# Kernel optimization log

Measured on AMD Instinct MI355X. Metric: run time of the kernel, lower is better.

## Reference

```python
import jax, jax.numpy as jnp
import numpy as np

D = 2            # stalk dimension d
FD = 3           # final_d = d + 1 (add_lp=True, add_hp=False)
HID = 32         # hidden_channels
N_NODES = 50000
E0 = 200000      # undirected edges; directed edge list has 2*E0 entries (second half reversed)
IN_CH = 128
OUT_CH = 32
N_LAYERS = 2
PSIZE = D * (D + 1) // 2  # cayley param size per edge


def _spectral_normalize(W, iters=20):
    # torch spectral_norm: power iteration with detached u, v; sigma = u^T W v
    u = jnp.full((W.shape[0],), 1.0 / np.sqrt(W.shape[0]), W.dtype)
    def body(_, u):
        v = W.T @ u
        v = v / (jnp.linalg.norm(v) + 1e-12)
        u2 = W @ v
        return u2 / (jnp.linalg.norm(u2) + 1e-12)
    u = jax.lax.fori_loop(0, iters, body, u)
    u = jax.lax.stop_gradient(u)
    v = jax.lax.stop_gradient(W.T @ u)
    v = v / (jnp.linalg.norm(v) + 1e-12)
    return W / (u @ W @ v)


def _cayley(p):
    # p: [E, PSIZE] lower-tri params -> skew A -> orthogonal Q = (I - A)^{-1}(I + A)
    E = p.shape[0]
    r, c = jnp.tril_indices(D)
    M = jnp.zeros((E, D, D), p.dtype).at[:, r, c].set(p)
    A = M - jnp.swapaxes(M, 1, 2)
    I = jnp.eye(D, dtype=p.dtype)
    return jnp.linalg.solve(I[None] - A, I[None] + A)


def setup_inputs() -> dict:
    key = jax.random.key(0)
    ks = jax.random.split(key, 8)
    src = jax.random.randint(ks[0], (E0,), 0, N_NODES)
    dst = jax.random.randint(ks[1], (E0,), 0, N_NODES)
    # symmetric directed edge list; edge j and edge j+E0 are reverses of each other
    edge_index = jnp.concatenate([jnp.stack([src, dst]), jnp.stack([dst, src])], axis=1)
    x = jax.random.normal(ks[2], (N_NODES, IN_CH), jnp.float32)
    s = 0.02
    W1 = jax.random.normal(ks[3], (FD * HID, IN_CH), jnp.float32) * s
    b1 = jnp.zeros((FD * HID,), jnp.float32)
    W2 = jax.random.normal(ks[4], (OUT_CH, FD * HID), jnp.float32) * s
    b2 = jnp.zeros((OUT_CH,), jnp.float32)
    W_left = jnp.tile(jnp.eye(FD, dtype=jnp.float32)[None], (N_LAYERS, 1, 1))  # init eye per torch
    W_right = jax.random.normal(ks[5], (N_LAYERS, HID, HID), jnp.float32) / np.sqrt(HID)
    eps = jnp.zeros((N_LAYERS, FD, 1), jnp.float32)
    W_sheaf = jax.random.normal(ks[6], (N_LAYERS, PSIZE, 2 * FD * HID), jnp.float32) * s
    W_wt = jax.random.normal(ks[7], (N_LAYERS, 1, 2 * FD * HID), jnp.float32) * s
    return {"x": x, "edge_index": edge_index, "W1": W1, "b1": b1, "W2": W2, "b2": b2,
            "W_left": W_left, "W_right": W_right, "eps": eps, "W_sheaf": W_sheaf, "W_wt": W_wt}


def reference(x, edge_index, W1, b1, W2, b2, W_left, W_right, eps, W_sheaf, W_wt):
    N = x.shape[0]
    row, col = edge_index[0], edge_index[1]
    e0 = row.shape[0] // 2
    rev = jnp.concatenate([jnp.arange(e0) + e0, jnp.arange(e0)])  # reverse-edge index
    # lin1 + ELU (dropouts = 0 in eval)
    h = jax.nn.elu(x @ W1.T + b1)                 # [N, FD*HID]
    xc = h.reshape(N * FD, HID)                   # [N*FD, HID]
    x0 = xc
    for layer in range(N_LAYERS):
        # --- sheaf learner + edge weight learner (gather endpoint features) ---
        xn = xc.reshape(N, FD * HID)
        cat = jnp.concatenate([xn[row], xn[col]], axis=-1)   # [2*E0, 2*FD*HID]
        p = jnp.tanh(cat @ W_sheaf[layer].T)                 # sheaf map params [2*E0, PSIZE]
        wdir = jax.nn.sigmoid(cat @ W_wt[layer].T)[:, 0]
        w = wdir * wdir[rev]                                 # symmetric edge weight
        # --- normalized connection (bundle) Laplacian ---
        Q = _cayley(p)                                       # per-edge orthogonal maps
        T = jnp.einsum('eij,eik->ejk', Q, Q[rev])            # transport F_u^T F_v
        w2 = w * w
        deg = jax.ops.segment_sum(w2, row, num_segments=N)
        dinv = jnp.where(deg > 0, jax.lax.rsqrt(jnp.maximum(deg, 1e-30)), 0.0)
        cnorm = w2 * dinv[row] * dinv[col]                   # [2*E0]
        # --- left / right weights (spectral-normalized) ---
        Wl = _spectral_normalize(W_left[layer])
        Wr = _spectral_normalize(W_right[layer])
        y = xc.reshape(N, FD, HID)
        y = jnp.einsum('ef,nfh->neh', Wl, y)                 # mix stalk dims
        y = jnp.einsum('neh,ch->nec', y, Wr)                 # mix channels
        # --- apply block-sparse Laplacian: Lx[u] = x[u] - sum_e c_e B_e x[v] ---
        yv = y[col]                                          # gather  [2*E0, FD, HID]
        tv = jnp.concatenate([jnp.einsum('eij,ejh->eih', T, yv[:, :D]), yv[:, D:]], axis=1)
        agg = jax.ops.segment_sum(cnorm[:, None, None] * tv, row, num_segments=N)
        diag = jnp.where(deg > 0, 1.0, 0.0)[:, None, None]
        z = jax.nn.elu((diag * y - agg).reshape(N * FD, HID))
        # --- epsilon-gated residual ---
        coeff = jnp.tile(1.0 + jnp.tanh(eps[layer]), (N, 1))  # [N*FD, 1]
        x0 = coeff * x0 - z
        xc = x0
    return xc.reshape(N, FD * HID) @ W2.T + b2
```

## Files before the change

kernel.cpp:

```cpp
#include <hip/hip_runtime.h>

#define NN 50000
#define E0 200000
#define E2 400000
#define NGROUPS ((NN + 7) / 8)
#define NCHUNK  ((NN + 255) / 256)
#define NTILES  ((NN + 63) / 64)
#define EB      ((E2 + 255) / 256)

typedef __attribute__((ext_vector_type(8))) short short8;
typedef __attribute__((ext_vector_type(4))) float f32x4;

__device__ __forceinline__ float eluf(float x) { return x > 0.0f ? x : expm1f(x); }
__device__ __forceinline__ float fsig(float x) { return 1.0f / (1.0f + __expf(-x)); }
__device__ __forceinline__ float ftanh(float x) {
    float e = __expf(-2.0f * x);
    return (1.0f - e) / (1.0f + e);
}
__device__ __forceinline__ unsigned rne_bf16(float x) {
    unsigned u = __float_as_uint(x);
    return (u + 0x7fffu + ((u >> 16) & 1u)) >> 16;
}

__device__ __forceinline__ void spectral_block(int l, const float* __restrict__ Wl_in,
                                               const float* __restrict__ Wr_in,
                                               float* __restrict__ Wl_out, float* __restrict__ Wr_out) {
    __shared__ float W[32 * 33];
    __shared__ float sscal;
    int t = threadIdx.x;
    for (int i = t; i < 1024; i += 256) W[(i >> 5) * 33 + (i & 31)] = Wr_in[l * 1024 + i];
    __syncthreads();
    if (t < 32) {
        float u = 0.17677669529663688f;
        for (int it = 0; it < 20; ++it) {
            float v = 0.f;
#pragma unroll 8
            for (int r = 0; r < 32; ++r) v = fmaf(W[r * 33 + t], __shfl(u, r, 32), v);
            float s = v * v;
#pragma unroll
            for (int off = 16; off; off >>= 1) s += __shfl_xor(s, off, 32);
            v *= 1.0f / (sqrtf(s) + 1e-12f);
            float u2 = 0.f;
#pragma unroll 8
            for (int c = 0; c < 32; ++c) u2 = fmaf(W[t * 33 + c], __shfl(v, c, 32), u2);
            s = u2 * u2;
#pragma unroll
            for (int off = 16; off; off >>= 1) s += __shfl_xor(s, off, 32);
            u = u2 * (1.0f / (sqrtf(s) + 1e-12f));
        }
        float v = 0.f;
#pragma unroll 8
        for (int r = 0; r < 32; ++r) v = fmaf(W[r * 33 + t], __shfl(u, r, 32), v);
        float s = v * v;
#pragma unroll
        for (int off = 16; off; off >>= 1) s += __shfl_xor(s, off, 32);
        if (t == 0) sscal = (sqrtf(s) + 1e-12f) / s;
    } else if (t == 64) {
        float M[9];
        for (int i = 0; i < 9; ++i) M[i] = Wl_in[l * 9 + i];
        float u[3] = {0.5773502691896258f, 0.5773502691896258f, 0.5773502691896258f};
        float v[3], u2[3];
        for (int it = 0; it < 20; ++it) {
            float s = 0;
            for (int c = 0; c < 3; ++c) { v[c] = M[c] * u[0] + M[3 + c] * u[1] + M[6 + c] * u[2]; s += v[c] * v[c]; }
            float inv = 1.0f / (sqrtf(s) + 1e-12f);
            for (int c = 0; c < 3; ++c) v[c] *= inv;
            s = 0;
            for (int r = 0; r < 3; ++r) { u2[r] = M[r * 3] * v[0] + M[r * 3 + 1] * v[1] + M[r * 3 + 2] * v[2]; s += u2[r] * u2[r]; }
            inv = 1.0f / (sqrtf(s) + 1e-12f);
            for (int r = 0; r < 3; ++r) u[r] = u2[r] * inv;
        }
        float s = 0;
        for (int c = 0; c < 3; ++c) { v[c] = M[c] * u[0] + M[3 + c] * u[1] + M[6 + c] * u[2]; s += v[c] * v[c]; }
        float inv = (sqrtf(s) + 1e-12f) / s;
        for (int i = 0; i < 9; ++i) Wl_out[l * 9 + i] = M[i] * inv;
    }
    __syncthreads();
    float invs = sscal;
    for (int i = t; i < 1024; i += 256) Wr_out[l * 1024 + i] = W[(i >> 5) * 33 + (i & 31)] * invs;
}

__global__ __launch_bounds__(256) void k_setup(const float* __restrict__ Wl_in, const float* __restrict__ Wr_in,
                                               float* __restrict__ Wl_out, float* __restrict__ Wr_out,
                                               int* __restrict__ cnt, int* __restrict__ fill,
                                               float* __restrict__ deg0, int* __restrict__ gtotal) {
    if (blockIdx.x < 2) {
        spectral_block((int)blockIdx.x, Wl_in, Wr_in, Wl_out, Wr_out);
        return;
    }
    int i = (blockIdx.x - 2) * 256 + threadIdx.x;
    if (i == 0) *gtotal = 0;
    if (i < NN) { cnt[i] = 0; fill[i] = 0; deg0[i] = 0.0f; }
}

template<int K, int N, int NH, bool ELU, bool HIST>
__global__ __launch_bounds__(256) void k_gemm(const float* __restrict__ X,
                                              const float* __restrict__ W,
                                              const float* __restrict__ bias,
                                              float* __restrict__ out,
                                              const int* __restrict__ row, int* __restrict__ cnt) {
    constexpr int KP = K + 8;
    constexpr int NT = NH / 16;
    constexpr int KS = K / 32;
    constexpr int NHALVES = N / NH;
    __shared__ __align__(16) unsigned short whi[NH * KP];
    __shared__ __align__(16) unsigned short wlo[NH * KP];
    int tid = threadIdx.x;
    if (HIST) {
        for (int e = blockIdx.x * 256 + tid; e < E2; e += gridDim.x * 256)
            atomicAdd(&cnt[row[e]], 1);
    }
    const int ch = blockIdx.x % NHALVES;
    const int tstream = blockIdx.x / NHALVES;
    const int nstreams = gridDim.x / NHALVES;
    for (int i = tid; i < NH * K; i += 256) {
        float v = W[ch * NH * K + i];
        int r = i / K, c = i % K;
        unsigned h = rne_bf16(v);
        whi[r * KP + c] = (unsigned short)h;
        wlo[r * KP + c] = (unsigned short)rne_bf16(v - __uint_as_float(h << 16));
    }
    __syncthreads();
    int wave = tid >> 6, lane = tid & 63;
    int quad = lane >> 4, r16 = lane & 15;
    for (int t = tstream; t < NTILES; t += nstreams) {
        long m = (long)t * 64 + wave * 16 + r16;
        long mc = m < NN ? m : (NN - 1);
        const float* xrow = X + mc * K + quad * 8;
        short8 ah[KS], al[KS];
#pragma unroll
        for (int ks = 0; ks < KS; ++ks) {
            const float4* xp = (const float4*)(xrow + ks * 32);
            float4 p0 = xp[0], p1 = xp[1];
            float xv[8] = {p0.x, p0.y, p0.z, p0.w, p1.x, p1.y, p1.z, p1.w};
#pragma unroll
            for (int j = 0; j < 8; ++j) {
                unsigned h = rne_bf16(xv[j]);
                ah[ks][j] = (short)h;
                al[ks][j] = (short)rne_bf16(xv[j] - __uint_as_float(h << 16));
            }
        }
        long mbase = (long)t * 64 + wave * 16 + quad * 4;
#pragma unroll
        for (int tt = 0; tt < NT; ++tt) {
            f32x4 acc = (f32x4){0.f, 0.f, 0.f, 0.f};
#pragma unroll
            for (int ks = 0; ks < KS; ++ks) {
                int ro = (tt * 16 + r16) * KP + ks * 32 + quad * 8;
                short8 bh = *(const short8*)&whi[ro];
                short8 bl = *(const short8*)&wlo[ro];
                acc = __builtin_amdgcn_mfma_f32_16x16x32_bf16(ah[ks], bh, acc, 0, 0, 0);
                acc = __builtin_amdgcn_mfma_f32_16x16x32_bf16(al[ks], bh, acc, 0, 0, 0);
                acc = __builtin_amdgcn_mfma_f32_16x16x32_bf16(ah[ks], bl, acc, 0, 0, 0);
            }
            int coln = ch * NH + tt * 16 + r16;
            float b = bias[coln];
#pragma unroll
            for (int rr = 0; rr < 4; ++rr) {
                long mm = mbase + rr;
                if (mm < NN) {
                    float v = acc[rr] + b;
                    if (ELU) v = eluf(v);
                    out[mm * N + coln] = v;
                }
            }
        }
    }
}

__global__ __launch_bounds__(256) void k_scan(const int* __restrict__ cnt, int* __restrict__ start,
                                              int* __restrict__ gtotal) {
    __shared__ int s[256];
    __shared__ int soff;
    int b = blockIdx.x, t = threadIdx.x;
    int i = b * 256 + t;
    int v = (i < NN) ? cnt[i] : 0;
    s[t] = v;
    __syncthreads();
    for (int off = 1; off < 256; off <<= 1) {
        int add = (t >= off) ? s[t - off] : 0;
        __syncthreads();
        s[t] += add;
        __syncthreads();
    }
    if (t == 255) soff = atomicAdd(gtotal, s[255]);
    __syncthreads();
    if (i < NN) start[i] = s[t] - v + soff;
}

__global__ __launch_bounds__(256) void k_filly8(const float* __restrict__ xc,
                                                const float* __restrict__ Wl, const float* __restrict__ Wr,
                                                const float* __restrict__ Wsh, const float* __restrict__ Wwt,
                                                unsigned* __restrict__ yA, unsigned short* __restrict__ yB,
                                                float4* __restrict__ proj,
                                                const int* __restrict__ row, const int* __restrict__ start,
                                                int* __restrict__ fill, int* __restrict__ eslot) {
    int tid = threadIdx.x;
    if (blockIdx.x >= NGROUPS) {
        int e = (blockIdx.x - NGROUPS) * 256 + tid;
        if (e < E2) {
            int u = row[e];
            eslot[e] = start[u] + atomicAdd(&fill[u], 1);
        }
        return;
    }
    __shared__ float wrs[32 * 33];
    __shared__ float wls[9];
    __shared__ float xcs[8][96];
    __shared__ float ws1[192], wt[192];
    int n0 = blockIdx.x * 8;
    for (int i = tid; i < 1024; i += 256) wrs[(i >> 5) * 33 + (i & 31)] = Wr[i];
    if (tid < 9) wls[tid] = Wl[tid];
    if (tid < 192) {
        ws1[tid] = Wsh[192 + tid];
        wt[tid]  = Wwt[tid];
    }
    for (int i = tid; i < 192; i += 256) {
        int nd = i / 24, of = (i % 24) * 4;
        *(float4*)&xcs[nd][of] = *(const float4*)&xc[(n0 + nd) * 96 + of];
    }
    __syncthreads();
    int node = tid >> 5, c = tid & 31;
    int n = n0 + node;
    float a1 = 0, a2 = 0, a3 = 0, a4 = 0;
#pragma unroll
    for (int j = 0; j < 3; ++j) {
        int k = j * 32 + c;
        float xv = xcs[node][k];
        a1 = fmaf(xv, ws1[k], a1);
        a2 = fmaf(xv, ws1[96 + k], a2);
        a3 = fmaf(xv, wt[k], a3);
        a4 = fmaf(xv, wt[96 + k], a4);
    }
#pragma unroll
    for (int off = 16; off; off >>= 1) {
        a1 += __shfl_xor(a1, off);
        a2 += __shfl_xor(a2, off);
        a3 += __shfl_xor(a3, off);
        a4 += __shfl_xor(a4, off);
    }
    if (c == 0) proj[n] = make_float4(a1, a2, a3, a4);
    {
        float t0 = 0, t1 = 0, t2 = 0;
        const float* wr = &wrs[c * 33];
        const float* xr = xcs[node];
#pragma unroll
        for (int h = 0; h < 32; ++h) {
            float w = wr[h];
            t0 = fmaf(xr[h], w, t0);
            t1 = fmaf(xr[32 + h], w, t1);
            t2 = fmaf(xr[64 + h], w, t2);
        }
        float o0 = wls[0] * t0 + wls[1] * t1 + wls[2] * t2;
        float o1 = wls[3] * t0 + wls[4] * t1 + wls[5] * t2;
        float o2 = wls[6] * t0 + wls[7] * t1 + wls[8] * t2;
        yA[n * 32 + c] = rne_bf16(o0) | (rne_bf16(o1) << 16);
        yB[n * 32 + c] = (unsigned short)rne_bf16(o2);
    }
}

__global__ __launch_bounds__(256) void k_coef(const int* __restrict__ row, const int* __restrict__ col,
                                              const int* __restrict__ eslot,
                                              const float4* __restrict__ proj,
                                              uint2* __restrict__ meta, float* __restrict__ deg) {
    int e = blockIdx.x * 256 + threadIdx.x;
    if (e >= E0) return;
    int u = row[e], v = col[e];
    float4 pu = proj[u], pv = proj[v];
    float a_e = ftanh(pu.x + pv.y);
    float a_r = ftanh(pv.x + pu.y);
    float wd_e = fsig(pu.z + pv.w);
    float wd_r = fsig(pv.z + pu.w);
    float w = wd_e * wd_r;
    float w2 = w * w;
    float ie = 1.0f / (1.0f + a_e * a_e), ir = 1.0f / (1.0f + a_r * a_r);
    float ce = (1.0f - a_e * a_e) * ie, se = 2.0f * a_e * ie;
    float cr = (1.0f - a_r * a_r) * ir, sr = 2.0f * a_r * ir;
    float C = ce * cr + se * sr;
    float S = ce * sr - se * cr;
    unsigned cb = rne_bf16(C), sb = rne_bf16(S), wb = rne_bf16(w2);
    meta[eslot[e]]      = make_uint2(cb | (sb << 16), (unsigned)v | (wb << 16));
    meta[eslot[e + E0]] = make_uint2(cb | ((sb ^ 0x8000u) << 16), (unsigned)u | (wb << 16));
    atomicAdd(&deg[u], w2);
    atomicAdd(&deg[v], w2);
}

__device__ __forceinline__ void gather_accum(int s0, int ec, int c,
                                             const uint2* __restrict__ meta,
                                             const float* __restrict__ deg, float du,
                                             const unsigned* __restrict__ yA,
                                             const unsigned short* __restrict__ yB,
                                             float4* __restrict__ ecoef,
                                             float& acc0, float& acc1, float& acc2) {
    for (int bs = 0; bs < ec; bs += 32) {
        int nb2 = min(32, ec - bs);
        if (c < nb2) {
            uint2 mt = meta[s0 + bs + c];
            int vj = (int)(mt.y & 0xffffu);
            float w2 = __uint_as_float(mt.y & 0xffff0000u);
            float Cv = __uint_as_float(mt.x << 16);
            float Sv = __uint_as_float(mt.x & 0xffff0000u);
            float dv = deg[vj];
            float dvi = dv > 0.0f ? rsqrtf(fmaxf(dv, 1e-30f)) : 0.0f;
            float cnl = w2 * du * dvi;
            ecoef[c] = make_float4(cnl * Cv, cnl * Sv, cnl, __int_as_float(vj));
        }
        int j4 = nb2 & ~3;
        int j = 0;
        for (; j < j4; j += 4) {
#pragma unroll
            for (int jj = 0; jj < 4; ++jj) {
                float4 e = ecoef[j + jj];
                int v = __float_as_int(e.w);
                unsigned ua = yA[v * 32 + c];
                unsigned ub = (unsigned)yB[v * 32 + c];
                float y0 = __uint_as_float(ua << 16);
                float y1 = __uint_as_float(ua & 0xffff0000u);
                float y2 = __uint_as_float(ub << 16);
                acc0 = fmaf(e.x, y0, acc0);
                acc0 = fmaf(-e.y, y1, acc0);
                acc1 = fmaf(e.y, y0, acc1);
                acc1 = fmaf(e.x, y1, acc1);
                acc2 = fmaf(e.z, y2, acc2);
            }
        }
        for (; j < nb2; ++j) {
            float4 e = ecoef[j];
            int v = __float_as_int(e.w);
            unsigned ua = yA[v * 32 + c];
            unsigned ub = (unsigned)yB[v * 32 + c];
            float y0 = __uint_as_float(ua << 16);
            float y1 = __uint_as_float(ua & 0xffff0000u);
            float y2 = __uint_as_float(ub << 16);
            acc0 = fmaf(e.x, y0, acc0);
            acc0 = fmaf(-e.y, y1, acc0);
            acc1 = fmaf(e.y, y0, acc1);
            acc1 = fmaf(e.x, y1, acc1);
            acc2 = fmaf(e.z, y2, acc2);
        }
    }
}

__global__ __launch_bounds__(256) void k_gatherY(const int* __restrict__ start,
                                                 const int* __restrict__ cnt,
                                                 const uint2* __restrict__ meta,
                                                 const float* __restrict__ deg0,
                                                 const unsigned* __restrict__ yA0,
                                                 const unsigned short* __restrict__ yB0,
                                                 const float* __restrict__ eps,
                                                 float* __restrict__ xc,
                                                 const float* __restrict__ Wl, const float* __restrict__ Wr,
                                                 const float* __restrict__ Wsh, const float* __restrict__ Wwt,
                                                 unsigned* __restrict__ yA1, unsigned short* __restrict__ yB1,
                                                 float4* __restrict__ proj, float* __restrict__ deg1) {
    __shared__ float wrs[32 * 33];
    __shared__ float wls[9];
    __shared__ float xcs[8][96];
    __shared__ float ws1[192], wt[192];
    __shared__ float4 ecoef[8][32];
    int tid = threadIdx.x;
    int node = tid >> 5, c = tid & 31;
    int n = blockIdx.x * 8 + node;
    int s0 = start[n], ec = cnt[n];
    float dn = deg0[n];
    for (int i = tid; i < 1024; i += 256) wrs[(i >> 5) * 33 + (i & 31)] = Wr[i];
    if (tid < 9) wls[tid] = Wl[tid];
    if (tid < 192) {
        ws1[tid] = Wsh[(1 * 3 + 1) * 192 + tid];
        wt[tid]  = Wwt[1 * 192 + tid];
    }
    __syncthreads();
    float du = dn > 0.0f ? rsqrtf(fmaxf(dn, 1e-30f)) : 0.0f;
    float acc0 = 0, acc1 = 0, acc2 = 0;
    gather_accum(s0, ec, c, meta, deg0, du, yA0, yB0, ecoef[node], acc0, acc1, acc2);
    float diag = dn > 0.0f ? 1.0f : 0.0f;
    unsigned ua = yA0[n * 32 + c];
    unsigned ub = (unsigned)yB0[n * 32 + c];
    float oy0 = __uint_as_float(ua << 16);
    float oy1 = __uint_as_float(ua & 0xffff0000u);
    float oy2 = __uint_as_float(ub << 16);
    float c0 = 1.0f + tanhf(eps[0]);
    float c1 = 1.0f + tanhf(eps[1]);
    float c2 = 1.0f + tanhf(eps[2]);
    int base = n * 96 + c;
    float nx0 = c0 * xc[base]      - eluf(diag * oy0 - acc0);
    float nx1 = c1 * xc[base + 32] - eluf(diag * oy1 - acc1);
    float nx2 = c2 * xc[base + 64] - eluf(diag * oy2 - acc2);
    xc[base] = nx0; xc[base + 32] = nx1; xc[base + 64] = nx2;
    if (c == 0) deg1[n] = 0.0f;
    xcs[node][c] = nx0; xcs[node][32 + c] = nx1; xcs[node][64 + c] = nx2;
    float a1 = nx0 * ws1[c] + nx1 * ws1[32 + c] + nx2 * ws1[64 + c];
    float a2 = nx0 * ws1[96 + c] + nx1 * ws1[128 + c] + nx2 * ws1[160 + c];
    float a3 = nx0 * wt[c] + nx1 * wt[32 + c] + nx2 * wt[64 + c];
    float a4 = nx0 * wt[96 + c] + nx1 * wt[128 + c] + nx2 * wt[160 + c];
#pragma unroll
    for (int off = 16; off; off >>= 1) {
        a1 += __shfl_xor(a1, off);
        a2 += __shfl_xor(a2, off);
        a3 += __shfl_xor(a3, off);
        a4 += __shfl_xor(a4, off);
    }
    if (c == 0) proj[n] = make_float4(a1, a2, a3, a4);
    {
        float t0 = 0, t1 = 0, t2 = 0;
        const float* wr = &wrs[c * 33];
        const float* xr = xcs[node];
#pragma unroll
        for (int h = 0; h < 32; ++h) {
            float w = wr[h];
            t0 = fmaf(xr[h], w, t0);
            t1 = fmaf(xr[32 + h], w, t1);
            t2 = fmaf(xr[64 + h], w, t2);
        }
        float o0 = wls[0] * t0 + wls[1] * t1 + wls[2] * t2;
        float o1 = wls[3] * t0 + wls[4] * t1 + wls[5] * t2;
        float o2 = wls[6] * t0 + wls[7] * t1 + wls[8] * t2;
        yA1[n * 32 + c] = rne_bf16(o0) | (rne_bf16(o1) << 16);
        yB1[n * 32 + c] = (unsigned short)rne_bf16(o2);
    }
}

__global__ __launch_bounds__(256) void k_gather(const int* __restrict__ start,
                                                const int* __restrict__ cnt,
                                                const uint2* __restrict__ meta,
                                                const float* __restrict__ deg,
                                                const unsigned* __restrict__ yA,
                                                const unsigned short* __restrict__ yB,
                                                const float* __restrict__ eps,
                                                int layer, float* __restrict__ xc) {
    __shared__ float4 ecoef[8][32];
    int tid = threadIdx.x;
    int node = tid >> 5, c = tid & 31;
    int n = blockIdx.x * 8 + node;
    if (n >= NN) return;
    int s0 = start[n], ec = cnt[n];
    float dn = deg[n];
    float du = dn > 0.0f ? rsqrtf(fmaxf(dn, 1e-30f)) : 0.0f;
    float acc0 = 0, acc1 = 0, acc2 = 0;
    gather_accum(s0, ec, c, meta, deg, du, yA, yB, ecoef[node], acc0, acc1, acc2);
    float diag = dn > 0.0f ? 1.0f : 0.0f;
    unsigned ua = yA[n * 32 + c];
    unsigned ub = (unsigned)yB[n * 32 + c];
    float oy0 = __uint_as_float(ua << 16);
    float oy1 = __uint_as_float(ua & 0xffff0000u);
    float oy2 = __uint_as_float(ub << 16);
    float c0 = 1.0f + tanhf(eps[layer * 3 + 0]);
    float c1 = 1.0f + tanhf(eps[layer * 3 + 1]);
    float c2 = 1.0f + tanhf(eps[layer * 3 + 2]);
    int base = n * 96 + c;
    float z0 = eluf(diag * oy0 - acc0);
    float z1 = eluf(diag * oy1 - acc1);
    float z2 = eluf(diag * oy2 - acc2);
    xc[base]      = c0 * xc[base]      - z0;
    xc[base + 32] = c1 * xc[base + 32] - z1;
    xc[base + 64] = c2 * xc[base + 64] - z2;
}

extern "C" void kernel_launch(void* const* d_in, const int* in_sizes, int n_in,
                              void* d_out, int out_size, void* d_ws, size_t ws_size,
                              hipStream_t stream) {
    const float* x     = (const float*)d_in[0];
    const int*   ei    = (const int*)d_in[1];
    const float* W1    = (const float*)d_in[2];
    const float* b1    = (const float*)d_in[3];
    const float* W2    = (const float*)d_in[4];
    const float* b2    = (const float*)d_in[5];
    const float* Wl    = (const float*)d_in[6];
    const float* Wr    = (const float*)d_in[7];
    const float* eps   = (const float*)d_in[8];
    const float* Wsh   = (const float*)d_in[9];
    const float* Wwt   = (const float*)d_in[10];
    float* out = (float*)d_out;
    const int* row = ei;
    const int* col = ei + E2;

    char* pc = (char*)d_ws;
    float* xc     = (float*)pc;          pc += (size_t)NN * 96 * 4;
    uint2* meta   = (uint2*)pc;          pc += (size_t)E2 * 8;
    unsigned* yA0 = (unsigned*)pc;       pc += (size_t)NN * 32 * 4;
    unsigned* yA1 = (unsigned*)pc;       pc += (size_t)NN * 32 * 4;
    unsigned short* yB0 = (unsigned short*)pc; pc += (size_t)NN * 32 * 2;
    unsigned short* yB1 = (unsigned short*)pc; pc += (size_t)NN * 32 * 2;
    pc = (char*)(((size_t)pc + 15) & ~(size_t)15);
    float4* proj  = (float4*)pc;         pc += (size_t)NN * 16;
    float* deg0   = (float*)pc;          pc += (size_t)NN * 4;
    float* deg1   = (float*)pc;          pc += (size_t)NN * 4;
    float* Wl_n   = (float*)pc;          pc += 32 * 4;
    float* Wr_n   = (float*)pc;          pc += 2048 * 4;
    int* cnt      = (int*)pc;            pc += (size_t)NN * 4;
    int* start    = (int*)pc;            pc += (size_t)NN * 4;
    int* fill     = (int*)pc;            pc += (size_t)NN * 4;
    int* eslot    = (int*)pc;            pc += (size_t)E2 * 4;
    int* gtotal   = (int*)pc;            pc += 4;

    k_setup<<<NCHUNK + 2, 256, 0, stream>>>(Wl, Wr, Wl_n, Wr_n, cnt, fill, deg0, gtotal);
    k_gemm<128, 96, 48, true, true><<<1024, 256, 0, stream>>>(x, W1, b1, xc, row, cnt);
    k_scan<<<NCHUNK, 256, 0, stream>>>(cnt, start, gtotal);
    k_filly8<<<NGROUPS + EB, 256, 0, stream>>>(xc, Wl_n, Wr_n, Wsh, Wwt,
                                               yA0, yB0, proj, row, start, fill, eslot);
    k_coef<<<(E0 + 255) / 256, 256, 0, stream>>>(row, col, eslot, proj, meta, deg0);
    k_gatherY<<<NGROUPS, 256, 0, stream>>>(start, cnt, meta, deg0, yA0, yB0, eps, xc,
                                           Wl_n + 9, Wr_n + 1024, Wsh, Wwt, yA1, yB1, proj, deg1);
    k_coef<<<(E0 + 255) / 256, 256, 0, stream>>>(row, col, eslot, proj, meta, deg1);
    k_gather<<<NGROUPS, 256, 0, stream>>>(start, cnt, meta, deg1, yA1, yB1, eps, 1, xc);
    k_gemm<96, 32, 32, false, false><<<782, 256, 0, stream>>>(xc, W2, b2, out, nullptr, nullptr);
}
```

Before: 316.9 us.

## Fold layer-0 left/right weights into one matrix and compute y via MFMA GEMM

Precomputes, in the setup kernel, a combined 112x96 matrix that holds the Kronecker product of the normalized left and right weights plus the sheaf and weight projection rows for layer 0. It then replaces the scalar per-node k_filly8 kernel with an MFMA bf16 split-precision GEMM that produces y and the projections in one pass. This moves the layer-0 feature transform from FMA loops on the vector units onto matrix cores. In exchange it does extra padded work (112 output columns) and adds bf16 split-precision rounding error.

```diff
diff --git a/kernel.cpp b/kernel.cpp
--- a/kernel.cpp
+++ b/kernel.cpp
@@ -24,9 +24,12 @@
 
 __device__ __forceinline__ void spectral_block(int l, const float* __restrict__ Wl_in,
                                                const float* __restrict__ Wr_in,
-                                               float* __restrict__ Wl_out, float* __restrict__ Wr_out) {
+                                               float* __restrict__ Wl_out, float* __restrict__ Wr_out,
+                                               const float* __restrict__ Wsh, const float* __restrict__ Wwt,
+                                               float* __restrict__ M0) {
     __shared__ float W[32 * 33];
     __shared__ float sscal;
+    __shared__ float wl_s[9];
     int t = threadIdx.x;
     for (int i = t; i < 1024; i += 256) W[(i >> 5) * 33 + (i & 31)] = Wr_in[l * 1024 + i];
     __syncthreads();
@@ -73,19 +76,34 @@
         float s = 0;
         for (int c = 0; c < 3; ++c) { v[c] = M[c] * u[0] + M[3 + c] * u[1] + M[6 + c] * u[2]; s += v[c] * v[c]; }
         float inv = (sqrtf(s) + 1e-12f) / s;
-        for (int i = 0; i < 9; ++i) Wl_out[l * 9 + i] = M[i] * inv;
+        for (int i = 0; i < 9; ++i) { float w = M[i] * inv; Wl_out[l * 9 + i] = w; wl_s[i] = w; }
     }
     __syncthreads();
     float invs = sscal;
     for (int i = t; i < 1024; i += 256) Wr_out[l * 1024 + i] = W[(i >> 5) * 33 + (i & 31)] * invs;
+    if (l == 0) {
+        for (int i = t; i < 96 * 96; i += 256) {
+            int yc = i / 96, k = i % 96;
+            int e = yc >> 5, cc = yc & 31, f = k >> 5, h = k & 31;
+            M0[yc * 96 + k] = wl_s[e * 3 + f] * W[cc * 33 + h] * invs;
+        }
+        for (int i = t; i < 4 * 96; i += 256) {
+            int r = i / 96, k = i % 96;
+            float v = (r < 2) ? Wsh[192 + r * 96 + k] : Wwt[(r - 2) * 96 + k];
+            M0[(96 + r) * 96 + k] = v;
+        }
+        for (int i = t; i < 12 * 96; i += 256) M0[100 * 96 + i] = 0.f;
+    }
 }
 
 __global__ __launch_bounds__(256) void k_setup(const float* __restrict__ Wl_in, const float* __restrict__ Wr_in,
                                                float* __restrict__ Wl_out, float* __restrict__ Wr_out,
+                                               const float* __restrict__ Wsh, const float* __restrict__ Wwt,
+                                               float* __restrict__ M0,
                                                int* __restrict__ cnt, int* __restrict__ fill,
                                                float* __restrict__ deg0, int* __restrict__ gtotal) {
     if (blockIdx.x < 2) {
-        spectral_block((int)blockIdx.x, Wl_in, Wr_in, Wl_out, Wr_out);
+        spectral_block((int)blockIdx.x, Wl_in, Wr_in, Wl_out, Wr_out, Wsh, Wwt, M0);
         return;
     }
     int i = (blockIdx.x - 2) * 256 + threadIdx.x;
@@ -168,6 +186,82 @@
     }
 }
 
+__global__ __launch_bounds__(256) void k_ygemm(const float* __restrict__ X,
+                                               const float* __restrict__ M,
+                                               unsigned* __restrict__ yA, unsigned short* __restrict__ yB,
+                                               float4* __restrict__ proj,
+                                               const int* __restrict__ row, const int* __restrict__ start,
+                                               int* __restrict__ fill, int* __restrict__ eslot) {
+    constexpr int K = 96, KP = 104, NH = 112, NT = 7, KS = 3;
+    int tid = threadIdx.x;
+    if (blockIdx.x >= NTILES) {
+        int e = (blockIdx.x - NTILES) * 256 + tid;
+        if (e < E2) {
+            int u = row[e];
+            eslot[e] = start[u] + atomicAdd(&fill[u], 1);
+        }
+        return;
+    }
+    __shared__ __align__(16) unsigned short whi[NH * KP];
+    __shared__ __align__(16) unsigned short wlo[NH * KP];
+    for (int i = tid; i < NH * K; i += 256) {
+        float v = M[i];
+        int r = i / K, c = i % K;
+        unsigned h = rne_bf16(v);
+        whi[r * KP + c] = (unsigned short)h;
+        wlo[r * KP + c] = (unsigned short)rne_bf16(v - __uint_as_float(h << 16));
+    }
+    __syncthreads();
+    int wave = tid >> 6, lane = tid & 63;
+    int quad = lane >> 4, r16 = lane & 15;
+    int t = blockIdx.x;
+    long m = (long)t * 64 + wave * 16 + r16;
+    long mc = m < NN ? m : (NN - 1);
+    const float* xrow = X + mc * K + quad * 8;
+    short8 ah[KS], al[KS];
+#pragma unroll
+    for (int ks = 0; ks < KS; ++ks) {
+        const float4* xp = (const float4*)(xrow + ks * 32);
+        float4 p0 = xp[0], p1 = xp[1];
+        float xv[8] = {p0.x, p0.y, p0.z, p0.w, p1.x, p1.y, p1.z, p1.w};
+#pragma unroll
+        for (int j = 0; j < 8; ++j) {
+            unsigned h = rne_bf16(xv[j]);
+            ah[ks][j] = (short)h;
+            al[ks][j] = (short)rne_bf16(xv[j] - __uint_as_float(h << 16));
+        }
+    }
+    f32x4 acc[NT];
+#pragma unroll
+    for (int tt = 0; tt < NT; ++tt) acc[tt] = (f32x4){0.f, 0.f, 0.f, 0.f};
+#pragma unroll
+    for (int tt = 0; tt < NT; ++tt) {
+#pragma unroll
+        for (int ks = 0; ks < KS; ++ks) {
+            int ro = (tt * 16 + r16) * KP + ks * 32 + quad * 8;
+            short8 bh = *(const short8*)&whi[ro];
+            short8 bl = *(const short8*)&wlo[ro];
+            acc[tt] = __builtin_amdgcn_mfma_f32_16x16x32_bf16(ah[ks], bh, acc[tt], 0, 0, 0);
+            acc[tt] = __builtin_amdgcn_mfma_f32_16x16x32_bf16(al[ks], bh, acc[tt], 0, 0, 0);
+            acc[tt] = __builtin_amdgcn_mfma_f32_16x16x32_bf16(ah[ks], bl, acc[tt], 0, 0, 0);
+        }
+    }
+    long mbase = (long)t * 64 + wave * 16 + quad * 4;
+#pragma unroll
+    for (int rr = 0; rr < 4; ++rr) {
+        long mm = mbase + rr;
+        if (mm < NN) {
+#pragma unroll
+            for (int tt = 0; tt < 2; ++tt) {
+                int c = tt * 16 + r16;
+                yA[mm * 32 + c] = rne_bf16(acc[tt][rr]) | (rne_bf16(acc[tt + 2][rr]) << 16);
+                yB[mm * 32 + c] = (unsigned short)rne_bf16(acc[tt + 4][rr]);
+            }
+            if (r16 < 4) ((float*)proj)[mm * 4 + r16] = acc[6][rr];
+        }
+    }
+}
+
 __global__ __launch_bounds__(256) void k_scan(const int* __restrict__ cnt, int* __restrict__ start,
                                               int* __restrict__ gtotal) {
     __shared__ int s[256];
@@ -186,77 +280,6 @@
     if (t == 255) soff = atomicAdd(gtotal, s[255]);
     __syncthreads();
     if (i < NN) start[i] = s[t] - v + soff;
-}
-
-__global__ __launch_bounds__(256) void k_filly8(const float* __restrict__ xc,
-                                                const float* __restrict__ Wl, const float* __restrict__ Wr,
-                                                const float* __restrict__ Wsh, const float* __restrict__ Wwt,
-                                                unsigned* __restrict__ yA, unsigned short* __restrict__ yB,
-                                                float4* __restrict__ proj,
-                                                const int* __restrict__ row, const int* __restrict__ start,
-                                                int* __restrict__ fill, int* __restrict__ eslot) {
-    int tid = threadIdx.x;
-    if (blockIdx.x >= NGROUPS) {
-        int e = (blockIdx.x - NGROUPS) * 256 + tid;
-        if (e < E2) {
-            int u = row[e];
-            eslot[e] = start[u] + atomicAdd(&fill[u], 1);
-        }
-        return;
-    }
-    __shared__ float wrs[32 * 33];
-    __shared__ float wls[9];
-    __shared__ float xcs[8][96];
-    __shared__ float ws1[192], wt[192];
-    int n0 = blockIdx.x * 8;
-    for (int i = tid; i < 1024; i += 256) wrs[(i >> 5) * 33 + (i & 31)] = Wr[i];
-    if (tid < 9) wls[tid] = Wl[tid];
-    if (tid < 192) {
-        ws1[tid] = Wsh[192 + tid];
-        wt[tid]  = Wwt[tid];
-    }
-    for (int i = tid; i < 192; i += 256) {
-        int nd = i / 24, of = (i % 24) * 4;
-        *(float4*)&xcs[nd][of] = *(const float4*)&xc[(n0 + nd) * 96 + of];
-    }
-    __syncthreads();
-    int node = tid >> 5, c = tid & 31;
-    int n = n0 + node;
-    float a1 = 0, a2 = 0, a3 = 0, a4 = 0;
-#pragma unroll
-    for (int j = 0; j < 3; ++j) {
-        int k = j * 32 + c;
-        float xv = xcs[node][k];
-        a1 = fmaf(xv, ws1[k], a1);
-        a2 = fmaf(xv, ws1[96 + k], a2);
-        a3 = fmaf(xv, wt[k], a3);
-        a4 = fmaf(xv, wt[96 + k], a4);
-    }
-#pragma unroll
-    for (int off = 16; off; off >>= 1) {
-        a1 += __shfl_xor(a1, off);
-        a2 += __shfl_xor(a2, off);
-        a3 += __shfl_xor(a3, off);
-        a4 += __shfl_xor(a4, off);
-    }
-    if (c == 0) proj[n] = make_float4(a1, a2, a3, a4);
-    {
-        float t0 = 0, t1 = 0, t2 = 0;
-        const float* wr = &wrs[c * 33];
-        const float* xr = xcs[node];
-#pragma unroll
-        for (int h = 0; h < 32; ++h) {
-            float w = wr[h];
-            t0 = fmaf(xr[h], w, t0);
-            t1 = fmaf(xr[32 + h], w, t1);
-            t2 = fmaf(xr[64 + h], w, t2);
-        }
-        float o0 = wls[0] * t0 + wls[1] * t1 + wls[2] * t2;
-        float o1 = wls[3] * t0 + wls[4] * t1 + wls[5] * t2;
-        float o2 = wls[6] * t0 + wls[7] * t1 + wls[8] * t2;
-        yA[n * 32 + c] = rne_bf16(o0) | (rne_bf16(o1) << 16);
-        yB[n * 32 + c] = (unsigned short)rne_bf16(o2);
-    }
 }
 
 __global__ __launch_bounds__(256) void k_coef(const int* __restrict__ row, const int* __restrict__ col,
@@ -487,17 +510,18 @@
     float* deg1   = (float*)pc;          pc += (size_t)NN * 4;
     float* Wl_n   = (float*)pc;          pc += 32 * 4;
     float* Wr_n   = (float*)pc;          pc += 2048 * 4;
+    float* M0     = (float*)pc;          pc += (size_t)112 * 96 * 4;
     int* cnt      = (int*)pc;            pc += (size_t)NN * 4;
     int* start    = (int*)pc;            pc += (size_t)NN * 4;
     int* fill     = (int*)pc;            pc += (size_t)NN * 4;
     int* eslot    = (int*)pc;            pc += (size_t)E2 * 4;
     int* gtotal   = (int*)pc;            pc += 4;
 
-    k_setup<<<NCHUNK + 2, 256, 0, stream>>>(Wl, Wr, Wl_n, Wr_n, cnt, fill, deg0, gtotal);
+    k_setup<<<NCHUNK + 2, 256, 0, stream>>>(Wl, Wr, Wl_n, Wr_n, Wsh, Wwt, M0,
+                                            cnt, fill, deg0, gtotal);
     k_gemm<128, 96, 48, true, true><<<1024, 256, 0, stream>>>(x, W1, b1, xc, row, cnt);
     k_scan<<<NCHUNK, 256, 0, stream>>>(cnt, start, gtotal);
-    k_filly8<<<NGROUPS + EB, 256, 0, stream>>>(xc, Wl_n, Wr_n, Wsh, Wwt,
-                                               yA0, yB0, proj, row, start, fill, eslot);
+    k_ygemm<<<NTILES + EB, 256, 0, stream>>>(xc, M0, yA0, yB0, proj, row, start, fill, eslot);
     k_coef<<<(E0 + 255) / 256, 256, 0, stream>>>(row, col, eslot, proj, meta, deg0);
     k_gatherY<<<NGROUPS, 256, 0, stream>>>(start, cnt, meta, deg0, yA0, yB0, eps, xc,
                                            Wl_n + 9, Wr_n + 1024, Wsh, Wwt, yA1, yB1, proj, deg1);
```

New measurement: 309.4 us. -2.4%, faster.
